# Performance work log

Measured on AMD Instinct MI355X. Metric: run time of the kernel, lower is better.

The kernel has to match this reference:

```python
import jax, jax.numpy as jnp
import numpy as np

N = 50000       # num nodes
E = 800000      # num edges
F_NODE = 128    # input node feature dim
F_EDGE = 32     # input edge feature dim
H = 64          # hidden dim (heads=1)
NEG_SLOPE = 0.2 # GAT leaky-relu slope


def _segment_softmax(scores, seg, num_segments):
    # numerically stable softmax over edges grouped by destination node
    m = jax.ops.segment_max(scores, seg, num_segments=num_segments)
    ex = jnp.exp(scores - m[seg])
    denom = jax.ops.segment_sum(ex, seg, num_segments=num_segments)
    return ex / (denom[seg] + 1e-16)


def _egat_conv(x, src, dst, eattr, W, We, a_src, a_dst, a_e, b):
    # PyG-style GAT layer with edge features (heads=1, no self loops).
    xp = x @ W                      # [N, H] projected nodes
    ep = eattr @ We                 # [E, H] projected edges (returned as new edge feats)
    score = (xp @ a_src)[src] + (xp @ a_dst)[dst] + ep @ a_e  # [E]
    score = jax.nn.leaky_relu(score, NEG_SLOPE)
    alpha = _segment_softmax(score, dst, N)                    # [E]
    out = jax.ops.segment_sum(alpha[:, None] * xp[src], dst, num_segments=N) + b
    return out, alpha, ep


def setup_inputs() -> dict:
    key = jax.random.key(0)
    ks = jax.random.split(key, 24)
    inp = {
        "x": jax.random.normal(ks[0], (N, F_NODE), jnp.float32),
        "edge_index": jax.random.randint(ks[1], (2, E), 0, N, jnp.int64),
        "edge_attr": jax.random.normal(ks[2], (E, F_EDGE), jnp.float32),
    }
    def glorot(k, shape):
        fan = shape[0] + shape[-1]
        return jax.random.normal(k, shape, jnp.float32) * jnp.sqrt(2.0 / fan)
    dims = [(F_NODE, F_EDGE), (H, H), (H, H)]
    i = 3
    for li, (din, dedge) in enumerate(dims, start=1):
        inp[f"W{li}"] = glorot(ks[i], (din, H)); i += 1
        inp[f"We{li}"] = glorot(ks[i], (dedge, H)); i += 1
        inp[f"as{li}"] = glorot(ks[i], (H,)); i += 1
        inp[f"ad{li}"] = glorot(ks[i], (H,)); i += 1
        inp[f"ae{li}"] = glorot(ks[i], (H,)); i += 1
        inp[f"b{li}"] = jnp.zeros((H,), jnp.float32)
    inp["Wc"] = glorot(ks[i], (H, 1)); i += 1
    inp["bc"] = jnp.zeros((1,), jnp.float32)
    return inp


def reference(x, edge_index, edge_attr,
              W1, We1, as1, ad1, ae1, b1,
              W2, We2, as2, ad2, ae2, b2,
              W3, We3, as3, ad3, ae3, b3,
              Wc, bc):
    src, dst = edge_index[0], edge_index[1]
    # layer 1 (edge feats projected F_EDGE -> H, reused as next edge_attr)
    x1, _, e1 = _egat_conv(x, src, dst, edge_attr, W1, We1, as1, ad1, ae1, b1)
    x1 = jax.nn.relu(x1)  # dropout is identity in eval mode
    # layer 2
    x2, _, e2 = _egat_conv(x1, src, dst, e1, W2, We2, as2, ad2, ae2, b2)
    x2 = jax.nn.relu(x2)
    # layer 3
    x3, _, _ = _egat_conv(x2, src, dst, e2, W3, We3, as3, ad3, ae3, b3)
    x3 = jax.nn.relu(x3)
    return x3 @ Wc + bc  # [N, 1]
```

## Files before the change

kernel.cpp:

```cpp
#include <hip/hip_runtime.h>
#include <hip/hip_fp16.h>
#include <math.h>

#define NN 50000
#define NE 800000
#define FN 128
#define FE 32
#define HD 64
#define NB 49
#define GP ((NN + 127) / 128)
#define GE ((NE + 255) / 256)

typedef unsigned long long u64;
typedef unsigned short u16;

__global__ void k_vecs_zero(const float* __restrict__ We1, const float* __restrict__ We2,
                            const float* __restrict__ We3, const float* __restrict__ ae1,
                            const float* __restrict__ ae2, const float* __restrict__ ae3,
                            float* __restrict__ v123, int* __restrict__ deg) {
  const int i = blockIdx.x * blockDim.x + threadIdx.x;
  if (i < NN) deg[i] = 0;
  if (blockIdx.x != 0) return;
  __shared__ float u2[HD], u3[HD], u23[HD];
  const int t = threadIdx.x;
  if (t < HD) {
    float s2 = 0.f, s3 = 0.f;
    for (int j = 0; j < HD; ++j) {
      s2 += We2[t * HD + j] * ae2[j];
      s3 += We3[t * HD + j] * ae3[j];
    }
    u2[t] = s2; u3[t] = s3;
  }
  __syncthreads();
  if (t < HD) {
    float s23 = 0.f;
    for (int j = 0; j < HD; ++j) s23 += We2[t * HD + j] * u3[j];
    u23[t] = s23;
  }
  __syncthreads();
  if (t < FE) {
    float a = 0.f, b = 0.f, c = 0.f;
    for (int j = 0; j < HD; ++j) {
      float w = We1[t * HD + j];
      a += w * ae1[j];
      b += w * u2[j];
      c += w * u23[j];
    }
    v123[t] = a; v123[32 + t] = b; v123[64 + t] = c;
  }
}

__global__ __launch_bounds__(256) void k_mega(
    const float* __restrict__ x, const float* __restrict__ W,
    const float* __restrict__ asv, const float* __restrict__ adv,
    __half* __restrict__ xph, float* __restrict__ ssrc, float* __restrict__ sdst,
    const int* __restrict__ srcA, const int* __restrict__ dstA,
    const float* __restrict__ eattr, const float* __restrict__ v123,
    int* __restrict__ deg, u16* __restrict__ rank, u64* __restrict__ trec) {
  __shared__ __half swh[FN * 64];
  __shared__ float sxT[32 * 128];
  const int t = threadIdx.x;
  if (blockIdx.x >= GP) {
    const int k = blockIdx.x - GP;
    const int e = (k >> 1) * 256 + t;
    if (e >= NE) return;
    if (k & 1) {
      rank[e] = (u16)atomicAdd(&deg[dstA[e]], 1);
    } else {
      const float4* ea = (const float4*)(eattr + (size_t)e * FE);
      float a = 0.f, b = 0.f, c = 0.f;
#pragma unroll
      for (int q = 0; q < FE / 4; ++q) {
        float4 xv = ea[q];
        const float* v1 = v123 + q * 4;
        const float* v2 = v123 + 32 + q * 4;
        const float* v3 = v123 + 64 + q * 4;
        a += xv.x * v1[0] + xv.y * v1[1] + xv.z * v1[2] + xv.w * v1[3];
        b += xv.x * v2[0] + xv.y * v2[1] + xv.z * v2[2] + xv.w * v2[3];
        c += xv.x * v3[0] + xv.y * v3[1] + xv.z * v3[2] + xv.w * v3[3];
      }
      trec[e] = (u64)(u16)srcA[e]
              | ((u64)__half_as_ushort(__float2half_rn(a)) << 16)
              | ((u64)__half_as_ushort(__float2half_rn(b)) << 32)
              | ((u64)__half_as_ushort(__float2half_rn(c)) << 48);
    }
    return;
  }
  const int w = t >> 6, l = t & 63;
  const int g = w * 4 + (l >> 4);
  const int r0 = g * 8;
  const int c0 = (l & 15) * 4;
  const int row0 = blockIdx.x * 128;

  for (int i = t; i < FN * 64; i += 256) swh[i] = __float2half_rn(W[i]);

  float acc[8][4];
#pragma unroll
  for (int i = 0; i < 8; ++i)
#pragma unroll
    for (int j = 0; j < 4; ++j) acc[i][j] = 0.f;

  for (int kt = 0; kt < FN; kt += 32) {
    __syncthreads();
#pragma unroll
    for (int pass = 0; pass < 4; ++pass) {
      int p = pass * 256 + t;
      int r = p >> 3, q = p & 7;
      int gr = row0 + r;
      float4 v = make_float4(0.f, 0.f, 0.f, 0.f);
      if (gr < NN) v = *(const float4*)(x + (size_t)gr * FN + kt + q * 4);
      sxT[(q * 4 + 0) * 128 + r] = v.x;
      sxT[(q * 4 + 1) * 128 + r] = v.y;
      sxT[(q * 4 + 2) * 128 + r] = v.z;
      sxT[(q * 4 + 3) * 128 + r] = v.w;
    }
    __syncthreads();
#pragma unroll
    for (int kk = 0; kk < 32; ++kk) {
      union { float2 f2; __half2 h2[2]; } ub;
      ub.f2 = *(const float2*)(swh + (kt + kk) * 64 + c0);
      float2 bb0 = __half22float2(ub.h2[0]);
      float2 bb1 = __half22float2(ub.h2[1]);
      float4 a0 = *(const float4*)(sxT + kk * 128 + r0);
      float4 a1 = *(const float4*)(sxT + kk * 128 + r0 + 4);
      float av[8] = {a0.x, a0.y, a0.z, a0.w, a1.x, a1.y, a1.z, a1.w};
      float bv[4] = {bb0.x, bb0.y, bb1.x, bb1.y};
#pragma unroll
      for (int i = 0; i < 8; ++i)
#pragma unroll
        for (int j = 0; j < 4; ++j) acc[i][j] += av[i] * bv[j];
    }
  }

  float as4[4], ad4[4];
#pragma unroll
  for (int j = 0; j < 4; ++j) { as4[j] = asv[c0 + j]; ad4[j] = adv[c0 + j]; }
#pragma unroll
  for (int i = 0; i < 8; ++i) {
    int gr = row0 + r0 + i;
    float ps = 0.f, pd = 0.f;
#pragma unroll
    for (int j = 0; j < 4; ++j) {
      ps += acc[i][j] * as4[j];
      pd += acc[i][j] * ad4[j];
    }
#pragma unroll
    for (int off = 1; off < 16; off <<= 1) {
      ps += __shfl_xor(ps, off);
      pd += __shfl_xor(pd, off);
    }
    if (gr < NN) {
      union { __half2 h2[2]; float2 f2; } u;
      u.h2[0] = __floats2half2_rn(acc[i][0], acc[i][1]);
      u.h2[1] = __floats2half2_rn(acc[i][2], acc[i][3]);
      *(float2*)(xph + (size_t)gr * HD + c0) = u.f2;
      if ((l & 15) == 0) { ssrc[gr] = ps; sdst[gr] = pd; }
    }
  }
}

__global__ __launch_bounds__(256) void k_scanA(const int* __restrict__ deg,
                                               int* __restrict__ bsum) {
  __shared__ int ws[4];
  const int t = threadIdx.x, lane = t & 63, wid = t >> 6;
  const int i0 = blockIdx.x * 1024 + t * 4;
  int s = 0;
#pragma unroll
  for (int j = 0; j < 4; ++j) {
    int i = i0 + j;
    if (i < NN) s += deg[i];
  }
#pragma unroll
  for (int off = 32; off; off >>= 1) s += __shfl_xor(s, off);
  if (lane == 0) ws[wid] = s;
  __syncthreads();
  if (t == 0) bsum[blockIdx.x] = ws[0] + ws[1] + ws[2] + ws[3];
}

__global__ __launch_bounds__(256) void k_scanB(const int* __restrict__ deg,
                                               const int* __restrict__ bsum,
                                               int* __restrict__ row_ptr) {
  __shared__ int blockOff;
  __shared__ int wOff[4];
  const int b = blockIdx.x;
  const int t = threadIdx.x, lane = t & 63, wid = t >> 6;
  if (t < 64) {
    int v = (t < NB) ? bsum[t] : 0;
    int p = v;
#pragma unroll
    for (int off = 1; off < 64; off <<= 1) {
      int u = __shfl_up(p, off);
      if (lane >= off) p += u;
    }
    if (t == b) blockOff = p - v;
    if (b == 0 && t == NB - 1) row_ptr[NN] = p;
  }
  __syncthreads();
  const int i0 = b * 1024 + t * 4;
  int v[4];
#pragma unroll
  for (int j = 0; j < 4; ++j) {
    int i = i0 + j;
    v[j] = (i < NN) ? deg[i] : 0;
  }
  int s = v[0] + v[1] + v[2] + v[3];
  int p = s;
#pragma unroll
  for (int off = 1; off < 64; off <<= 1) {
    int u = __shfl_up(p, off);
    if (lane >= off) p += u;
  }
  if (lane == 63) wOff[wid] = p;
  __syncthreads();
  int woff = 0;
  for (int wq = 0; wq < wid; ++wq) woff += wOff[wq];
  int excl = blockOff + woff + (p - s);
#pragma unroll
  for (int j = 0; j < 4; ++j) {
    int i = i0 + j;
    if (i < NN) row_ptr[i] = excl;
    excl += v[j];
  }
}

__global__ void k_scatter(const int* __restrict__ dstA, const u16* __restrict__ rank,
                          const int* __restrict__ row_ptr, const u64* __restrict__ trec,
                          u64* __restrict__ aos) {
  const int e = blockIdx.x * blockDim.x + threadIdx.x;
  if (e >= NE) return;
  aos[row_ptr[dstA[e]] + (int)rank[e]] = trec[e];
}

template <int TSEL>
__global__ __launch_bounds__(256) void k_agg_proj(
    const int* __restrict__ row_ptr, const u64* __restrict__ aos,
    const __half* __restrict__ xin, const float* __restrict__ ssrc_in,
    const float* __restrict__ sdst_in, const float* __restrict__ bias,
    const float* __restrict__ Wn, const float* __restrict__ asn,
    const float* __restrict__ adn, __half* __restrict__ xout,
    float* __restrict__ ssrc_out, float* __restrict__ sdst_out) {
  __shared__ __half swh[HD * HD];
  const int t = threadIdx.x;
  for (int i = t; i < HD * HD; i += 256) swh[i] = __float2half_rn(Wn[i]);

  const int gw = (blockIdx.x * blockDim.x + t) >> 6;
  const int lane = t & 63;
  const int g = lane >> 3;
  const int q = lane & 7;
  const int n = gw * 8 + g;
  const bool act = n < NN;
  int beg = 0, end = 0;
  float sd = 0.f;
  if (act) { beg = row_ptr[n]; end = row_ptr[n + 1]; sd = sdst_in[n]; }

  float dsum = 0.f;
  float4 o0 = make_float4(0.f, 0.f, 0.f, 0.f);
  float4 o1 = make_float4(0.f, 0.f, 0.f, 0.f);
  for (int base = beg; base < end; base += 16) {
    const int p0 = base + q, p1 = base + 8 + q;
    float pe0 = 0.f, pe1 = 0.f;
    int s0 = 0, s1 = 0;
    if (p0 < end) {
      u64 r = aos[p0];
      s0 = (int)(r & 0xFFFFu);
      float tt = __half2float(__ushort_as_half((u16)((r >> (16 * TSEL)) & 0xFFFFu)));
      float raw = ssrc_in[s0] + sd + tt;
      raw = raw > 0.f ? raw : 0.2f * raw;
      pe0 = __expf(raw);
    }
    if (p1 < end) {
      u64 r = aos[p1];
      s1 = (int)(r & 0xFFFFu);
      float tt = __half2float(__ushort_as_half((u16)((r >> (16 * TSEL)) & 0xFFFFu)));
      float raw = ssrc_in[s1] + sd + tt;
      raw = raw > 0.f ? raw : 0.2f * raw;
      pe1 = __expf(raw);
    }
    dsum += pe0 + pe1;
#pragma unroll
    for (int j = 0; j < 8; ++j) {
      const int sl = g * 8 + j;
      float pa = __shfl(pe0, sl);
      int sa = __shfl(s0, sl);
      float pb = __shfl(pe1, sl);
      int sb = __shfl(s1, sl);
      union { float4 f4; __half2 h2[4]; } ua, ub;
      ua.f4 = ((const float4*)(xin + (size_t)sa * HD))[q];
      ub.f4 = ((const float4*)(xin + (size_t)sb * HD))[q];
      float2 a0 = __half22float2(ua.h2[0]);
      float2 a1 = __half22float2(ua.h2[1]);
      float2 a2 = __half22float2(ua.h2[2]);
      float2 a3 = __half22float2(ua.h2[3]);
      o0.x += pa * a0.x; o0.y += pa * a0.y; o0.z += pa * a1.x; o0.w += pa * a1.y;
      o1.x += pa * a2.x; o1.y += pa * a2.y; o1.z += pa * a3.x; o1.w += pa * a3.y;
      float2 b0 = __half22float2(ub.h2[0]);
      float2 b1 = __half22float2(ub.h2[1]);
      float2 b2 = __half22float2(ub.h2[2]);
      float2 b3 = __half22float2(ub.h2[3]);
      o0.x += pb * b0.x; o0.y += pb * b0.y; o0.z += pb * b1.x; o0.w += pb * b1.y;
      o1.x += pb * b2.x; o1.y += pb * b2.y; o1.z += pb * b3.x; o1.w += pb * b3.y;
    }
  }
#pragma unroll
  for (int off = 1; off < 8; off <<= 1) dsum += __shfl_xor(dsum, off);

  const float inv = 1.f / (dsum + 1e-16f);
  const float4 b0 = ((const float4*)bias)[q * 2];
  const float4 b1 = ((const float4*)bias)[q * 2 + 1];
  float vreg[8];
  vreg[0] = fmaxf(o0.x * inv + b0.x, 0.f);
  vreg[1] = fmaxf(o0.y * inv + b0.y, 0.f);
  vreg[2] = fmaxf(o0.z * inv + b0.z, 0.f);
  vreg[3] = fmaxf(o0.w * inv + b0.w, 0.f);
  vreg[4] = fmaxf(o1.x * inv + b1.x, 0.f);
  vreg[5] = fmaxf(o1.y * inv + b1.y, 0.f);
  vreg[6] = fmaxf(o1.z * inv + b1.z, 0.f);
  vreg[7] = fmaxf(o1.w * inv + b1.w, 0.f);

  __syncthreads();

  float out8[8] = {0.f, 0.f, 0.f, 0.f, 0.f, 0.f, 0.f, 0.f};
#pragma unroll
  for (int kq = 0; kq < 8; ++kq) {
#pragma unroll
    for (int m = 0; m < 8; ++m) {
      float vb = __shfl(vreg[m], (lane & 56) | kq);
      union { float4 f4; __half2 h2[4]; } uw;
      uw.f4 = *(const float4*)(swh + (kq * 8 + m) * HD + q * 8);
      float2 w0 = __half22float2(uw.h2[0]);
      float2 w1 = __half22float2(uw.h2[1]);
      float2 w2 = __half22float2(uw.h2[2]);
      float2 w3 = __half22float2(uw.h2[3]);
      out8[0] += vb * w0.x; out8[1] += vb * w0.y;
      out8[2] += vb * w1.x; out8[3] += vb * w1.y;
      out8[4] += vb * w2.x; out8[5] += vb * w2.y;
      out8[6] += vb * w3.x; out8[7] += vb * w3.y;
    }
  }

  float ps = 0.f, pd = 0.f;
#pragma unroll
  for (int j = 0; j < 8; ++j) {
    ps += out8[j] * asn[q * 8 + j];
    pd += out8[j] * adn[q * 8 + j];
  }
#pragma unroll
  for (int off = 1; off < 8; off <<= 1) {
    ps += __shfl_xor(ps, off);
    pd += __shfl_xor(pd, off);
  }

  if (!act) return;
  union { float4 f4; __half2 h2[4]; } w;
  w.h2[0] = __floats2half2_rn(out8[0], out8[1]);
  w.h2[1] = __floats2half2_rn(out8[2], out8[3]);
  w.h2[2] = __floats2half2_rn(out8[4], out8[5]);
  w.h2[3] = __floats2half2_rn(out8[6], out8[7]);
  ((float4*)(xout + (size_t)n * HD))[q] = w.f4;
  if (q == 0) { ssrc_out[n] = ps; sdst_out[n] = pd; }
}

template <int TSEL>
__global__ __launch_bounds__(256) void k_agg_head(
    const int* __restrict__ row_ptr, const u64* __restrict__ aos,
    const __half* __restrict__ xin, const float* __restrict__ ssrc_in,
    const float* __restrict__ sdst_in, const float* __restrict__ bias,
    const float* __restrict__ Wc, const float* __restrict__ bc,
    float* __restrict__ outf) {
  const int gw = (blockIdx.x * blockDim.x + threadIdx.x) >> 6;
  const int lane = threadIdx.x & 63;
  const int g = lane >> 3;
  const int q = lane & 7;
  const int n = gw * 8 + g;
  const bool act = n < NN;
  int beg = 0, end = 0;
  float sd = 0.f;
  if (act) { beg = row_ptr[n]; end = row_ptr[n + 1]; sd = sdst_in[n]; }

  float dsum = 0.f;
  float4 o0 = make_float4(0.f, 0.f, 0.f, 0.f);
  float4 o1 = make_float4(0.f, 0.f, 0.f, 0.f);
  for (int base = beg; base < end; base += 16) {
    const int p0 = base + q, p1 = base + 8 + q;
    float pe0 = 0.f, pe1 = 0.f;
    int s0 = 0, s1 = 0;
    if (p0 < end) {
      u64 r = aos[p0];
      s0 = (int)(r & 0xFFFFu);
      float tt = __half2float(__ushort_as_half((u16)((r >> (16 * TSEL)) & 0xFFFFu)));
      float raw = ssrc_in[s0] + sd + tt;
      raw = raw > 0.f ? raw : 0.2f * raw;
      pe0 = __expf(raw);
    }
    if (p1 < end) {
      u64 r = aos[p1];
      s1 = (int)(r & 0xFFFFu);
      float tt = __half2float(__ushort_as_half((u16)((r >> (16 * TSEL)) & 0xFFFFu)));
      float raw = ssrc_in[s1] + sd + tt;
      raw = raw > 0.f ? raw : 0.2f * raw;
      pe1 = __expf(raw);
    }
    dsum += pe0 + pe1;
#pragma unroll
    for (int j = 0; j < 8; ++j) {
      const int sl = g * 8 + j;
      float pa = __shfl(pe0, sl);
      int sa = __shfl(s0, sl);
      float pb = __shfl(pe1, sl);
      int sb = __shfl(s1, sl);
      union { float4 f4; __half2 h2[4]; } ua, ub;
      ua.f4 = ((const float4*)(xin + (size_t)sa * HD))[q];
      ub.f4 = ((const float4*)(xin + (size_t)sb * HD))[q];
      float2 a0 = __half22float2(ua.h2[0]);
      float2 a1 = __half22float2(ua.h2[1]);
      float2 a2 = __half22float2(ua.h2[2]);
      float2 a3 = __half22float2(ua.h2[3]);
      o0.x += pa * a0.x; o0.y += pa * a0.y; o0.z += pa * a1.x; o0.w += pa * a1.y;
      o1.x += pa * a2.x; o1.y += pa * a2.y; o1.z += pa * a3.x; o1.w += pa * a3.y;
      float2 b0 = __half22float2(ub.h2[0]);
      float2 b1 = __half22float2(ub.h2[1]);
      float2 b2 = __half22float2(ub.h2[2]);
      float2 b3 = __half22float2(ub.h2[3]);
      o0.x += pb * b0.x; o0.y += pb * b0.y; o0.z += pb * b1.x; o0.w += pb * b1.y;
      o1.x += pb * b2.x; o1.y += pb * b2.y; o1.z += pb * b3.x; o1.w += pb * b3.y;
    }
  }
#pragma unroll
  for (int off = 1; off < 8; off <<= 1) dsum += __shfl_xor(dsum, off);

  if (!act) return;
  const float inv = 1.f / (dsum + 1e-16f);
  const float4 b0 = ((const float4*)bias)[q * 2];
  const float4 b1 = ((const float4*)bias)[q * 2 + 1];
  const float4 w0 = ((const float4*)Wc)[q * 2];
  const float4 w1 = ((const float4*)Wc)[q * 2 + 1];
  float c = fmaxf(o0.x * inv + b0.x, 0.f) * w0.x +
            fmaxf(o0.y * inv + b0.y, 0.f) * w0.y +
            fmaxf(o0.z * inv + b0.z, 0.f) * w0.z +
            fmaxf(o0.w * inv + b0.w, 0.f) * w0.w +
            fmaxf(o1.x * inv + b1.x, 0.f) * w1.x +
            fmaxf(o1.y * inv + b1.y, 0.f) * w1.y +
            fmaxf(o1.z * inv + b1.z, 0.f) * w1.z +
            fmaxf(o1.w * inv + b1.w, 0.f) * w1.w;
#pragma unroll
  for (int off = 1; off < 8; off <<= 1) c += __shfl_xor(c, off);
  if (q == 0) outf[n] = c + bc[0];
}

extern "C" void kernel_launch(void* const* d_in, const int* in_sizes, int n_in,
                              void* d_out, int out_size, void* d_ws, size_t ws_size,
                              hipStream_t stream) {
  const float* x     = (const float*)d_in[0];
  const int*   ei    = (const int*)d_in[1];
  const float* eattr = (const float*)d_in[2];
  const float* W1  = (const float*)d_in[3];
  const float* We1 = (const float*)d_in[4];
  const float* as1 = (const float*)d_in[5];
  const float* ad1 = (const float*)d_in[6];
  const float* ae1 = (const float*)d_in[7];
  const float* b1  = (const float*)d_in[8];
  const float* W2  = (const float*)d_in[9];
  const float* We2 = (const float*)d_in[10];
  const float* as2 = (const float*)d_in[11];
  const float* ad2 = (const float*)d_in[12];
  const float* ae2 = (const float*)d_in[13];
  const float* b2  = (const float*)d_in[14];
  const float* W3  = (const float*)d_in[15];
  const float* We3 = (const float*)d_in[16];
  const float* as3 = (const float*)d_in[17];
  const float* ad3 = (const float*)d_in[18];
  const float* ae3 = (const float*)d_in[19];
  const float* b3  = (const float*)d_in[20];
  const float* Wc  = (const float*)d_in[21];
  const float* bc  = (const float*)d_in[22];

  const int* srcA = ei;
  const int* dstA = ei + NE;
  float* outf = (float*)d_out;

  char* w = (char*)d_ws;
  auto alloc = [&](size_t bytes) {
    char* p = w;
    w += (bytes + 255) & ~(size_t)255;
    return p;
  };
  float* v123 = (float*)alloc(96 * 4);
  u64* aos = (u64*)alloc((size_t)NE * 8);
  u64* trec = (u64*)alloc((size_t)NE * 8);
  u16* rank = (u16*)alloc((size_t)NE * 2);
  int* row_ptr = (int*)alloc((size_t)(NN + 1) * 4);
  int* deg = (int*)alloc((size_t)NN * 4);
  int* bsum = (int*)alloc((size_t)NB * 4);
  __half* xpA = (__half*)alloc((size_t)NN * HD * 2);
  __half* xpB = (__half*)alloc((size_t)NN * HD * 2);
  float* ssrcA = (float*)alloc((size_t)NN * 4);
  float* sdstA = (float*)alloc((size_t)NN * 4);
  float* ssrcB = (float*)alloc((size_t)NN * 4);
  float* sdstB = (float*)alloc((size_t)NN * 4);

  const int gN = (NN + 255) / 256;
  const int gA = ((NN + 7) / 8 * 64 + 255) / 256;

  k_vecs_zero<<<gN, 256, 0, stream>>>(We1, We2, We3, ae1, ae2, ae3, v123, deg);
  k_mega<<<GP + 2 * GE, 256, 0, stream>>>(x, W1, as1, ad1, xpA, ssrcA, sdstA,
                                          srcA, dstA, eattr, v123, deg, rank, trec);
  k_scanA<<<NB, 256, 0, stream>>>(deg, bsum);
  k_scanB<<<NB, 256, 0, stream>>>(deg, bsum, row_ptr);
  k_scatter<<<GE, 256, 0, stream>>>(dstA, rank, row_ptr, trec, aos);
  k_agg_proj<1><<<gA, 256, 0, stream>>>(row_ptr, aos, xpA, ssrcA, sdstA, b1,
                                        W2, as2, ad2, xpB, ssrcB, sdstB);
  k_agg_proj<2><<<gA, 256, 0, stream>>>(row_ptr, aos, xpB, ssrcB, sdstB, b2,
                                        W3, as3, ad3, xpA, ssrcA, sdstA);
  k_agg_head<3><<<gA, 256, 0, stream>>>(row_ptr, aos, xpA, ssrcA, sdstA, b3,
                                        Wc, bc, outf);
}
```

Before: 148.3 us.

## Move layer-1 GEMM into scatter kernel and merge edge-degree/record work

Splits the old mega kernel: a new edge kernel does the degree atomics, the fp16 edge-score record packing and the rank write together, two edges per thread. The layer-1 node projection GEMM is moved into the scatter launch as extra blocks, rewritten without shared memory to read x and W directly from global memory in fp32. The goal is to shrink the pre-scan critical path and overlap the GEMM with the scatter. In exchange, the GEMM now relies on cache hits for repeated x and W loads instead of LDS tiling.

```diff
diff --git a/kernel.cpp b/kernel.cpp
--- a/kernel.cpp
+++ b/kernel.cpp
@@ -9,7 +9,7 @@
 #define HD 64
 #define NB 49
 #define GP ((NN + 127) / 128)
-#define GE ((NE + 255) / 256)
+#define EB ((NE + 511) / 512)
 
 typedef unsigned long long u64;
 typedef unsigned short u16;
@@ -50,113 +50,51 @@
   }
 }
 
-__global__ __launch_bounds__(256) void k_mega(
-    const float* __restrict__ x, const float* __restrict__ W,
-    const float* __restrict__ asv, const float* __restrict__ adv,
-    __half* __restrict__ xph, float* __restrict__ ssrc, float* __restrict__ sdst,
+__device__ __forceinline__ u64 make_trec(const float* __restrict__ eattr,
+                                         const float* __restrict__ v123,
+                                         int s, int e) {
+  const float4* ea = (const float4*)(eattr + (size_t)e * FE);
+  float a = 0.f, b = 0.f, c = 0.f;
+#pragma unroll
+  for (int q = 0; q < FE / 4; ++q) {
+    float4 xv = ea[q];
+    const float* v1 = v123 + q * 4;
+    const float* v2 = v123 + 32 + q * 4;
+    const float* v3 = v123 + 64 + q * 4;
+    a += xv.x * v1[0] + xv.y * v1[1] + xv.z * v1[2] + xv.w * v1[3];
+    b += xv.x * v2[0] + xv.y * v2[1] + xv.z * v2[2] + xv.w * v2[3];
+    c += xv.x * v3[0] + xv.y * v3[1] + xv.z * v3[2] + xv.w * v3[3];
+  }
+  return (u64)(u16)s
+       | ((u64)__half_as_ushort(__float2half_rn(a)) << 16)
+       | ((u64)__half_as_ushort(__float2half_rn(b)) << 32)
+       | ((u64)__half_as_ushort(__float2half_rn(c)) << 48);
+}
+
+__global__ __launch_bounds__(256, 8) void k_edge(
     const int* __restrict__ srcA, const int* __restrict__ dstA,
     const float* __restrict__ eattr, const float* __restrict__ v123,
     int* __restrict__ deg, u16* __restrict__ rank, u64* __restrict__ trec) {
-  __shared__ __half swh[FN * 64];
-  __shared__ float sxT[32 * 128];
   const int t = threadIdx.x;
-  if (blockIdx.x >= GP) {
-    const int k = blockIdx.x - GP;
-    const int e = (k >> 1) * 256 + t;
-    if (e >= NE) return;
-    if (k & 1) {
-      rank[e] = (u16)atomicAdd(&deg[dstA[e]], 1);
-    } else {
-      const float4* ea = (const float4*)(eattr + (size_t)e * FE);
-      float a = 0.f, b = 0.f, c = 0.f;
-#pragma unroll
-      for (int q = 0; q < FE / 4; ++q) {
-        float4 xv = ea[q];
-        const float* v1 = v123 + q * 4;
-        const float* v2 = v123 + 32 + q * 4;
-        const float* v3 = v123 + 64 + q * 4;
-        a += xv.x * v1[0] + xv.y * v1[1] + xv.z * v1[2] + xv.w * v1[3];
-        b += xv.x * v2[0] + xv.y * v2[1] + xv.z * v2[2] + xv.w * v2[3];
-        c += xv.x * v3[0] + xv.y * v3[1] + xv.z * v3[2] + xv.w * v3[3];
-      }
-      trec[e] = (u64)(u16)srcA[e]
-              | ((u64)__half_as_ushort(__float2half_rn(a)) << 16)
-              | ((u64)__half_as_ushort(__float2half_rn(b)) << 32)
-              | ((u64)__half_as_ushort(__float2half_rn(c)) << 48);
-    }
-    return;
-  }
-  const int w = t >> 6, l = t & 63;
-  const int g = w * 4 + (l >> 4);
-  const int r0 = g * 8;
-  const int c0 = (l & 15) * 4;
-  const int row0 = blockIdx.x * 128;
-
-  for (int i = t; i < FN * 64; i += 256) swh[i] = __float2half_rn(W[i]);
-
-  float acc[8][4];
-#pragma unroll
-  for (int i = 0; i < 8; ++i)
-#pragma unroll
-    for (int j = 0; j < 4; ++j) acc[i][j] = 0.f;
-
-  for (int kt = 0; kt < FN; kt += 32) {
-    __syncthreads();
-#pragma unroll
-    for (int pass = 0; pass < 4; ++pass) {
-      int p = pass * 256 + t;
-      int r = p >> 3, q = p & 7;
-      int gr = row0 + r;
-      float4 v = make_float4(0.f, 0.f, 0.f, 0.f);
-      if (gr < NN) v = *(const float4*)(x + (size_t)gr * FN + kt + q * 4);
-      sxT[(q * 4 + 0) * 128 + r] = v.x;
-      sxT[(q * 4 + 1) * 128 + r] = v.y;
-      sxT[(q * 4 + 2) * 128 + r] = v.z;
-      sxT[(q * 4 + 3) * 128 + r] = v.w;
-    }
-    __syncthreads();
-#pragma unroll
-    for (int kk = 0; kk < 32; ++kk) {
-      union { float2 f2; __half2 h2[2]; } ub;
-      ub.f2 = *(const float2*)(swh + (kt + kk) * 64 + c0);
-      float2 bb0 = __half22float2(ub.h2[0]);
-      float2 bb1 = __half22float2(ub.h2[1]);
-      float4 a0 = *(const float4*)(sxT + kk * 128 + r0);
-      float4 a1 = *(const float4*)(sxT + kk * 128 + r0 + 4);
-      float av[8] = {a0.x, a0.y, a0.z, a0.w, a1.x, a1.y, a1.z, a1.w};
-      float bv[4] = {bb0.x, bb0.y, bb1.x, bb1.y};
-#pragma unroll
-      for (int i = 0; i < 8; ++i)
-#pragma unroll
-        for (int j = 0; j < 4; ++j) acc[i][j] += av[i] * bv[j];
-    }
-  }
-
-  float as4[4], ad4[4];
-#pragma unroll
-  for (int j = 0; j < 4; ++j) { as4[j] = asv[c0 + j]; ad4[j] = adv[c0 + j]; }
-#pragma unroll
-  for (int i = 0; i < 8; ++i) {
-    int gr = row0 + r0 + i;
-    float ps = 0.f, pd = 0.f;
-#pragma unroll
-    for (int j = 0; j < 4; ++j) {
-      ps += acc[i][j] * as4[j];
-      pd += acc[i][j] * ad4[j];
-    }
-#pragma unroll
-    for (int off = 1; off < 16; off <<= 1) {
-      ps += __shfl_xor(ps, off);
-      pd += __shfl_xor(pd, off);
-    }
-    if (gr < NN) {
-      union { __half2 h2[2]; float2 f2; } u;
-      u.h2[0] = __floats2half2_rn(acc[i][0], acc[i][1]);
-      u.h2[1] = __floats2half2_rn(acc[i][2], acc[i][3]);
-      *(float2*)(xph + (size_t)gr * HD + c0) = u.f2;
-      if ((l & 15) == 0) { ssrc[gr] = ps; sdst[gr] = pd; }
-    }
-  }
+  const int base = blockIdx.x * 512;
+  const int e0 = base + t;
+  const int e1 = base + 256 + t;
+  const bool ok0 = e0 < NE, ok1 = e1 < NE;
+
+  int d0 = 0, d1 = 0, s0 = 0, s1 = 0;
+  if (ok0) d0 = dstA[e0];
+  if (ok1) d1 = dstA[e1];
+  int r0 = 0, r1 = 0;
+  if (ok0) r0 = atomicAdd(&deg[d0], 1);
+  if (ok1) r1 = atomicAdd(&deg[d1], 1);
+  if (ok0) s0 = srcA[e0];
+  if (ok1) s1 = srcA[e1];
+
+  if (ok0) trec[e0] = make_trec(eattr, v123, s0, e0);
+  if (ok1) trec[e1] = make_trec(eattr, v123, s1, e1);
+
+  if (ok0) rank[e0] = (u16)r0;
+  if (ok1) rank[e1] = (u16)r1;
 }
 
 __global__ __launch_bounds__(256) void k_scanA(const int* __restrict__ deg,
@@ -223,12 +161,82 @@
   }
 }
 
-__global__ void k_scatter(const int* __restrict__ dstA, const u16* __restrict__ rank,
-                          const int* __restrict__ row_ptr, const u64* __restrict__ trec,
-                          u64* __restrict__ aos) {
-  const int e = blockIdx.x * blockDim.x + threadIdx.x;
-  if (e >= NE) return;
-  aos[row_ptr[dstA[e]] + (int)rank[e]] = trec[e];
+__global__ __launch_bounds__(256, 6) void k_gemm_scatter(
+    const float* __restrict__ x, const float* __restrict__ W,
+    const float* __restrict__ asv, const float* __restrict__ adv,
+    __half* __restrict__ xph, float* __restrict__ ssrc, float* __restrict__ sdst,
+    const int* __restrict__ dstA, const u16* __restrict__ rank,
+    const int* __restrict__ row_ptr, const u64* __restrict__ trec,
+    u64* __restrict__ aos) {
+  const int t = threadIdx.x;
+  if (blockIdx.x >= GP) {
+    const int base = (blockIdx.x - GP) * 512;
+    const int e0 = base + t;
+    const int e1 = base + 256 + t;
+    if (e0 < NE) aos[row_ptr[dstA[e0]] + (int)rank[e0]] = trec[e0];
+    if (e1 < NE) aos[row_ptr[dstA[e1]] + (int)rank[e1]] = trec[e1];
+    return;
+  }
+  const int w = t >> 6, l = t & 63;
+  const int g = w * 4 + (l >> 4);
+  const int rr = g * 8;
+  const int c0 = (l & 15) * 4;
+  const int row0 = blockIdx.x * 128;
+
+  int xoff[8];
+#pragma unroll
+  for (int i = 0; i < 8; ++i) {
+    int gr = row0 + rr + i;
+    xoff[i] = (gr < NN ? gr : NN - 1) * FN;
+  }
+
+  float acc[8][4];
+#pragma unroll
+  for (int i = 0; i < 8; ++i)
+#pragma unroll
+    for (int j = 0; j < 4; ++j) acc[i][j] = 0.f;
+
+  for (int k = 0; k < FN; k += 4) {
+    float wv[4][4];
+#pragma unroll
+    for (int kk = 0; kk < 4; ++kk) {
+      float4 wq = *(const float4*)(W + (k + kk) * HD + c0);
+      wv[kk][0] = wq.x; wv[kk][1] = wq.y; wv[kk][2] = wq.z; wv[kk][3] = wq.w;
+    }
+#pragma unroll
+    for (int i = 0; i < 8; ++i) {
+      float4 a = *(const float4*)(x + xoff[i] + k);
+#pragma unroll
+      for (int j = 0; j < 4; ++j)
+        acc[i][j] += a.x * wv[0][j] + a.y * wv[1][j] + a.z * wv[2][j] + a.w * wv[3][j];
+    }
+  }
+
+  float as4[4], ad4[4];
+#pragma unroll
+  for (int j = 0; j < 4; ++j) { as4[j] = asv[c0 + j]; ad4[j] = adv[c0 + j]; }
+#pragma unroll
+  for (int i = 0; i < 8; ++i) {
+    int gr = row0 + rr + i;
+    float ps = 0.f, pd = 0.f;
+#pragma unroll
+    for (int j = 0; j < 4; ++j) {
+      ps += acc[i][j] * as4[j];
+      pd += acc[i][j] * ad4[j];
+    }
+#pragma unroll
+    for (int off = 1; off < 16; off <<= 1) {
+      ps += __shfl_xor(ps, off);
+      pd += __shfl_xor(pd, off);
+    }
+    if (gr < NN) {
+      union { __half2 h2[2]; float2 f2; } u;
+      u.h2[0] = __floats2half2_rn(acc[i][0], acc[i][1]);
+      u.h2[1] = __floats2half2_rn(acc[i][2], acc[i][3]);
+      *(float2*)(xph + (size_t)gr * HD + c0) = u.f2;
+      if ((l & 15) == 0) { ssrc[gr] = ps; sdst[gr] = pd; }
+    }
+  }
 }
 
 template <int TSEL>
@@ -351,12 +359,12 @@
   }
 
   if (!act) return;
-  union { float4 f4; __half2 h2[4]; } w;
-  w.h2[0] = __floats2half2_rn(out8[0], out8[1]);
-  w.h2[1] = __floats2half2_rn(out8[2], out8[3]);
-  w.h2[2] = __floats2half2_rn(out8[4], out8[5]);
-  w.h2[3] = __floats2half2_rn(out8[6], out8[7]);
-  ((float4*)(xout + (size_t)n * HD))[q] = w.f4;
+  union { float4 f4; __half2 h2[4]; } wv;
+  wv.h2[0] = __floats2half2_rn(out8[0], out8[1]);
+  wv.h2[1] = __floats2half2_rn(out8[2], out8[3]);
+  wv.h2[2] = __floats2half2_rn(out8[4], out8[5]);
+  wv.h2[3] = __floats2half2_rn(out8[6], out8[7]);
+  ((float4*)(xout + (size_t)n * HD))[q] = wv.f4;
   if (q == 0) { ssrc_out[n] = ps; sdst_out[n] = pd; }
 }
 
@@ -502,11 +510,11 @@
   const int gA = ((NN + 7) / 8 * 64 + 255) / 256;
 
   k_vecs_zero<<<gN, 256, 0, stream>>>(We1, We2, We3, ae1, ae2, ae3, v123, deg);
-  k_mega<<<GP + 2 * GE, 256, 0, stream>>>(x, W1, as1, ad1, xpA, ssrcA, sdstA,
-                                          srcA, dstA, eattr, v123, deg, rank, trec);
+  k_edge<<<EB, 256, 0, stream>>>(srcA, dstA, eattr, v123, deg, rank, trec);
   k_scanA<<<NB, 256, 0, stream>>>(deg, bsum);
   k_scanB<<<NB, 256, 0, stream>>>(deg, bsum, row_ptr);
-  k_scatter<<<GE, 256, 0, stream>>>(dstA, rank, row_ptr, trec, aos);
+  k_gemm_scatter<<<GP + EB, 256, 0, stream>>>(x, W1, as1, ad1, xpA, ssrcA, sdstA,
+                                              dstA, rank, row_ptr, trec, aos);
   k_agg_proj<1><<<gA, 256, 0, stream>>>(row_ptr, aos, xpA, ssrcA, sdstA, b1,
                                         W2, as2, ad2, xpB, ssrcB, sdstB);
   k_agg_proj<2><<<gA, 256, 0, stream>>>(row_ptr, aos, xpB, ssrcB, sdstB, b2,
```

After: 289.0 us. 1.95x slower.
